# Kernel tuning notes

Measured on AMD Instinct MI355X. Metric: run time of the kernel, lower is better.

Reference implementation:

```python
import jax, jax.numpy as jnp
import numpy as np

MAX_ITERS = 20
TOL = 1e-3


def best_fit_transform(A, B):
    # A, B: [N, m]; returns homogeneous transform T mapping A -> B.
    m = A.shape[1]
    cA = jnp.mean(A, axis=0)
    cB = jnp.mean(B, axis=0)
    AA = A - cA
    BB = B - cB
    H = AA.T @ BB                      # [m, m] cross-covariance
    U, S, Vt = jnp.linalg.svd(H)
    # reflection fix: if det(R) < 0, flip last row of Vt
    R0 = Vt.T @ U.T
    flip = jnp.linalg.det(R0) < 0
    Vt = Vt.at[m - 1].multiply(jnp.where(flip, -1.0, 1.0).astype(Vt.dtype))
    R = Vt.T @ U.T
    t = cB - R @ cA
    T = jnp.eye(m + 1, dtype=A.dtype).at[:m, :m].set(R).at[:m, m].set(t)
    return T, R, t


def nearest_neighbor(src, dst):
    # src, dst: [N, m]; brute-force 1-NN of each src point in dst.
    d2 = (jnp.sum(src * src, axis=1)[:, None]
          - 2.0 * (src @ dst.T)
          + jnp.sum(dst * dst, axis=1)[None, :])        # [N, N]
    idx = jnp.argmin(d2, axis=1)                          # [N]
    dmin = jnp.take_along_axis(d2, idx[:, None], axis=1)[:, 0]
    dist = jnp.sqrt(jnp.maximum(dmin, 0.0) + 1e-12)
    return dist, idx


def icp(A, B, max_iterations=MAX_ITERS, tolerance=TOL):
    m = A.shape[1]
    N = A.shape[0]
    src0 = jnp.concatenate([A.T, jnp.ones((1, N), A.dtype)], axis=0)  # [m+1, N]

    def step(carry, _):
        src, prev_err, done = carry
        dist, idx = nearest_neighbor(src[:m].T, B)
        T, _, _ = best_fit_transform(src[:m].T, B[idx])
        new_src = T @ src
        err = jnp.mean(dist)
        converged = jnp.abs(prev_err - err) < tolerance
        src = jnp.where(done, src, new_src)
        prev_err = jnp.where(done, prev_err, err)
        done = done | converged
        return (src, prev_err, done), None

    carry0 = (src0, jnp.zeros((), A.dtype), jnp.zeros((), bool))
    (src, _, _), _ = jax.lax.scan(step, carry0, None, length=max_iterations)
    T, _, _ = best_fit_transform(A, src[:m].T)
    return T


def setup_inputs() -> dict:
    key = jax.random.key(0)
    kA, kB = jax.random.split(key)
    A = jax.random.normal(kA, (8192, 3), dtype=jnp.float32)
    B = jax.random.normal(kB, (8192, 3), dtype=jnp.float32)
    return {"A": A, "B": B}


def reference(A, B):
    return icp(A, B)
```

## Files before the change

kernel.cpp:

```cpp
#include <hip/hip_runtime.h>

#define NPTS   8192
#define NB     256
#define NT     256
#define NSTEP  (NPTS / 64)
#define MAXIT  20
#define TOLER  1e-3
#define SPINCAP 200000000u

typedef unsigned long long u64;
typedef unsigned int u32;

#define WS_PART    0
#define WS_FLAGS   65536

__device__ inline double atom_ld(const double* p) {
  return __hip_atomic_load(p, __ATOMIC_RELAXED, __HIP_MEMORY_SCOPE_AGENT);
}
__device__ inline void atom_st(double* p, double v) {
  __hip_atomic_store(p, v, __ATOMIC_RELAXED, __HIP_MEMORY_SCOPE_AGENT);
}
__device__ inline int atom_ldi(const int* p) {
  return __hip_atomic_load(p, __ATOMIC_RELAXED, __HIP_MEMORY_SCOPE_AGENT);
}
__device__ inline void atom_sti(int* p, int v) {
  __hip_atomic_store(p, v, __ATOMIC_RELAXED, __HIP_MEMORY_SCOPE_AGENT);
}

__device__ void eig3_sym_desc(const double K[3][3], double w[3], double V[3][3])
{
  const double p1 = K[0][1]*K[0][1] + K[0][2]*K[0][2] + K[1][2]*K[1][2];
  const double q  = (K[0][0] + K[1][1] + K[2][2]) / 3.0;
  const double p2 = (K[0][0]-q)*(K[0][0]-q) + (K[1][1]-q)*(K[1][1]-q)
                  + (K[2][2]-q)*(K[2][2]-q) + 2.0*p1;
  if (p2 < 1e-280) {
    w[0]=w[1]=w[2]=q;
    V[0][0]=1;V[1][0]=0;V[2][0]=0; V[0][1]=0;V[1][1]=1;V[2][1]=0;
    V[0][2]=0;V[1][2]=0;V[2][2]=1;
    return;
  }
  const double p = sqrt(p2 / 6.0);
  const double ip = 1.0 / p;
  double Bm[3][3];
  for (int i = 0; i < 3; ++i)
    for (int j = 0; j < 3; ++j)
      Bm[i][j] = (K[i][j] - ((i==j) ? q : 0.0)) * ip;
  double detB = Bm[0][0]*(Bm[1][1]*Bm[2][2] - Bm[1][2]*Bm[2][1])
              - Bm[0][1]*(Bm[1][0]*Bm[2][2] - Bm[1][2]*Bm[2][0])
              + Bm[0][2]*(Bm[1][0]*Bm[2][1] - Bm[1][1]*Bm[2][0]);
  double r = detB * 0.5;
  r = (r < -1.0) ? -1.0 : ((r > 1.0) ? 1.0 : r);
  const double phi = acos(r) / 3.0;
  w[0] = q + 2.0*p*cos(phi);
  w[2] = q + 2.0*p*cos(phi + 2.0943951023931953);
  w[1] = 3.0*q - w[0] - w[2];
  for (int kk = 0; kk < 2; ++kk) {
    const int k = (kk == 0) ? 0 : 2;
    double lam = w[k];
    double r0[3] = {K[0][0]-lam, K[0][1], K[0][2]};
    double r1[3] = {K[1][0], K[1][1]-lam, K[1][2]};
    double r2[3] = {K[2][0], K[2][1], K[2][2]-lam};
    double c01[3] = {r0[1]*r1[2]-r0[2]*r1[1], r0[2]*r1[0]-r0[0]*r1[2], r0[0]*r1[1]-r0[1]*r1[0]};
    double c12[3] = {r1[1]*r2[2]-r1[2]*r2[1], r1[2]*r2[0]-r1[0]*r2[2], r1[0]*r2[1]-r1[1]*r2[0]};
    double c20[3] = {r2[1]*r0[2]-r2[2]*r0[1], r2[2]*r0[0]-r2[0]*r0[2]*0 - r2[0]*r0[2] + r2[2]*r0[0]*0, 0};
    c20[0] = r2[1]*r0[2] - r2[2]*r0[1];
    c20[1] = r2[2]*r0[0] - r2[0]*r0[2];
    c20[2] = r2[0]*r0[1] - r2[1]*r0[0];
    double n01 = c01[0]*c01[0]+c01[1]*c01[1]+c01[2]*c01[2];
    double n12 = c12[0]*c12[0]+c12[1]*c12[1]+c12[2]*c12[2];
    double n20 = c20[0]*c20[0]+c20[1]*c20[1]+c20[2]*c20[2];
    double* best = c01; double nb = n01;
    if (n12 > nb) { best = c12; nb = n12; }
    if (n20 > nb) { best = c20; nb = n20; }
    double inv = 1.0 / sqrt(nb + 1e-300);
    V[0][k]=best[0]*inv; V[1][k]=best[1]*inv; V[2][k]=best[2]*inv;
  }
  V[0][1] = V[1][2]*V[2][0] - V[2][2]*V[1][0];
  V[1][1] = V[2][2]*V[0][0] - V[0][2]*V[2][0];
  V[2][1] = V[0][2]*V[1][0] - V[1][2]*V[0][0];
  double nm = sqrt(V[0][1]*V[0][1]+V[1][1]*V[1][1]+V[2][1]*V[2][1]) + 1e-300;
  V[0][1] /= nm; V[1][1] /= nm; V[2][1] /= nm;
}

__device__ void kabsch_R(const double H[3][3], double R[3][3])
{
  double K[3][3];
  for (int i = 0; i < 3; ++i)
    for (int j = 0; j < 3; ++j) {
      double s = 0.0;
      for (int k = 0; k < 3; ++k) s += H[k][i] * H[k][j];
      K[i][j] = s;
    }
  double w[3], V[3][3];
  eig3_sym_desc(K, w, V);
  double U[3][3];
  for (int k = 0; k < 3; ++k) {
    double u0 = H[0][0]*V[0][k] + H[0][1]*V[1][k] + H[0][2]*V[2][k];
    double u1 = H[1][0]*V[0][k] + H[1][1]*V[1][k] + H[1][2]*V[2][k];
    double u2 = H[2][0]*V[0][k] + H[2][1]*V[1][k] + H[2][2]*V[2][k];
    double n = sqrt(u0*u0 + u1*u1 + u2*u2);
    if (n > 1e-150) { u0 /= n; u1 /= n; u2 /= n; }
    else if (k == 2) {
      u0 = U[1][0]*U[2][1] - U[2][0]*U[1][1];
      u1 = U[2][0]*U[0][1] - U[0][0]*U[2][1];
      u2 = U[0][0]*U[1][1] - U[1][0]*U[0][1];
      double n2 = sqrt(u0*u0 + u1*u1 + u2*u2) + 1e-300;
      u0 /= n2; u1 /= n2; u2 /= n2;
    } else {
      u0 = (k == 0) ? 1.0 : 0.0; u1 = (k == 1) ? 1.0 : 0.0; u2 = 0.0;
    }
    U[0][k] = u0; U[1][k] = u1; U[2][k] = u2;
  }
  double R0[3][3];
  for (int i = 0; i < 3; ++i)
    for (int j = 0; j < 3; ++j)
      R0[i][j] = V[i][0]*U[j][0] + V[i][1]*U[j][1] + V[i][2]*U[j][2];
  double det = R0[0][0]*(R0[1][1]*R0[2][2] - R0[1][2]*R0[2][1])
             - R0[0][1]*(R0[1][0]*R0[2][2] - R0[1][2]*R0[2][0])
             + R0[0][2]*(R0[1][0]*R0[2][1] - R0[1][1]*R0[2][0]);
  if (det < 0.0)
    for (int i = 0; i < 3; ++i)
      for (int j = 0; j < 3; ++j)
        R0[i][j] -= 2.0 * V[i][2] * U[j][2];
  for (int i = 0; i < 3; ++i)
    for (int j = 0; j < 3; ++j)
      R[i][j] = R0[i][j];
}

__global__ void icp_init(char* __restrict__ ws)
{
  ((int*)(ws + WS_FLAGS))[threadIdx.x] = 0;
}

__device__ inline void flag_barrier(int* flags, int blk, int gen,
                                    int tid, int wav, int lane)
{
  __syncthreads();
  if (tid == 0) {
    __threadfence();
    atom_sti(&flags[blk], gen);
  }
  if (wav == 0) {
    const int base = lane * 4;
    u32 spins = 0;
    bool ok = false;
    while (!ok && spins < SPINCAP) {
      int f0 = atom_ldi(&flags[base + 0]);
      int f1 = atom_ldi(&flags[base + 1]);
      int f2 = atom_ldi(&flags[base + 2]);
      int f3 = atom_ldi(&flags[base + 3]);
      ok = __all((f0 >= gen) && (f1 >= gen) && (f2 >= gen) && (f3 >= gen));
      ++spins;
    }
  }
  __syncthreads();
  __threadfence();
}

__global__ __launch_bounds__(NT, 1)
void icp_all(const float* __restrict__ A, const float* __restrict__ B,
             char* __restrict__ ws, float* __restrict__ out)
{
  double* partials = (double*)(ws + WS_PART);
  int*    flags    = (int*)(ws + WS_FLAGS);

  __shared__ __align__(16) float4 bp_lds[NPTS];
  __shared__ double red1[32 * 16];
  __shared__ double red2[4 * 16];
  __shared__ float  Tl[12];
  __shared__ int    dl;

  const int tid  = threadIdx.x;
  const int blk  = blockIdx.x;
  const int wav  = tid >> 6;
  const int lane = tid & 63;
  const int qbase = blk * 32 + wav * 8;

  for (int i = tid; i < NPTS; i += NT) {
    float bx = B[3*i], by = B[3*i+1], bz = B[3*i+2];
    bp_lds[i] = make_float4(2.f*bx, 2.f*by, 2.f*bz, bx*bx + by*by + bz*bz);
  }

  float ax[8], ay[8], az[8], sx[8], sy[8], sz[8];
  #pragma unroll
  for (int i = 0; i < 8; ++i) {
    int p = qbase + i;
    ax[i] = A[3*p]; ay[i] = A[3*p+1]; az[i] = A[3*p+2];
    sx[i] = ax[i];  sy[i] = ay[i];    sz[i] = az[i];
  }
  __syncthreads();

  double prev_err = 0.0;
  int it = 0;
  for (; it < MAXIT; ++it) {
    const int par = it & 1;
    float emin[8]; int imin[8];
    #pragma unroll
    for (int i = 0; i < 8; ++i) { emin[i] = 3.4e38f; imin[i] = 0; }

    float4 dcur = bp_lds[lane];
    #pragma unroll 4
    for (int stp = 0; stp < NSTEP - 1; ++stp) {
      float4 dnxt = bp_lds[(stp + 1) * 64 + lane];
      const int jg = stp * 64 + lane;
      #pragma unroll
      for (int i = 0; i < 8; ++i) {
        float e = fmaf(-sx[i], dcur.x, fmaf(-sy[i], dcur.y, fmaf(-sz[i], dcur.z, dcur.w)));
        if (e < emin[i]) { emin[i] = e; imin[i] = jg; }
      }
      dcur = dnxt;
    }
    {
      const int jg = (NSTEP - 1) * 64 + lane;
      #pragma unroll
      for (int i = 0; i < 8; ++i) {
        float e = fmaf(-sx[i], dcur.x, fmaf(-sy[i], dcur.y, fmaf(-sz[i], dcur.z, dcur.w)));
        if (e < emin[i]) { emin[i] = e; imin[i] = jg; }
      }
    }
    #pragma unroll
    for (int m = 1; m < 64; m <<= 1) {
      #pragma unroll
      for (int i = 0; i < 8; ++i) {
        float eo = __shfl_xor(emin[i], m, 64);
        int   io = __shfl_xor(imin[i], m, 64);
        if (eo < emin[i] || (eo == emin[i] && io < imin[i])) { emin[i] = eo; imin[i] = io; }
      }
    }

    #pragma unroll
    for (int i = 0; i < 8; ++i) {
      if (lane == i) {
        float s2 = sx[i]*sx[i] + sy[i]*sy[i] + sz[i]*sz[i];
        float d2 = emin[i] + s2;
        float dist = sqrtf(fmaxf(d2, 0.f) + 1e-12f);
        int j = imin[i];
        float bx = B[3*j], by = B[3*j+1], bz = B[3*j+2];
        double* r = red1 + (wav * 8 + i) * 16;
        r[0]=sx[i]; r[1]=sy[i]; r[2]=sz[i];
        r[3]=bx;    r[4]=by;    r[5]=bz;
        r[6]=(double)sx[i]*bx;  r[7]=(double)sx[i]*by;  r[8]=(double)sx[i]*bz;
        r[9]=(double)sy[i]*bx;  r[10]=(double)sy[i]*by; r[11]=(double)sy[i]*bz;
        r[12]=(double)sz[i]*bx; r[13]=(double)sz[i]*by; r[14]=(double)sz[i]*bz;
        r[15]=dist;
      }
    }
    __syncthreads();
    if (tid < 16) {
      double ssum = 0.0;
      for (int g = 0; g < 32; ++g) ssum += red1[g * 16 + tid];
      atom_st(&partials[((size_t)par * 16 + tid) * NB + blk], ssum);
    }
    flag_barrier(flags, blk, it + 1, tid, wav, lane);

    {
      double a2[16];
      #pragma unroll
      for (int k = 0; k < 16; ++k)
        a2[k] = atom_ld(&partials[((size_t)par * 16 + k) * NB + tid]);
      for (int m = 1; m < 64; m <<= 1) {
        #pragma unroll
        for (int k = 0; k < 16; ++k) a2[k] += __shfl_xor(a2[k], m, 64);
      }
      if (lane == 0)
        for (int k = 0; k < 16; ++k) red2[wav * 16 + k] = a2[k];
    }
    __syncthreads();
    if (tid == 0) {
      double S[16];
      for (int k = 0; k < 16; ++k)
        S[k] = red2[k] + red2[16+k] + red2[32+k] + red2[48+k];
      const double invN = 1.0 / NPTS;
      double cAv[3] = {S[0]*invN, S[1]*invN, S[2]*invN};
      double cBv[3] = {S[3]*invN, S[4]*invN, S[5]*invN};
      double H[3][3];
      for (int i = 0; i < 3; ++i)
        for (int j = 0; j < 3; ++j)
          H[i][j] = S[6 + i*3 + j] - (double)NPTS * cAv[i] * cBv[j];
      double err = S[15] * invN;
      int conv = (fabs(prev_err - err) < TOLER) ? 1 : 0;
      prev_err = err;
      double R[3][3];
      kabsch_R(H, R);
      double t0 = cBv[0] - (R[0][0]*cAv[0] + R[0][1]*cAv[1] + R[0][2]*cAv[2]);
      double t1 = cBv[1] - (R[1][0]*cAv[0] + R[1][1]*cAv[1] + R[1][2]*cAv[2]);
      double t2 = cBv[2] - (R[2][0]*cAv[0] + R[2][1]*cAv[1] + R[2][2]*cAv[2]);
      Tl[0]=(float)R[0][0]; Tl[1]=(float)R[0][1]; Tl[2]=(float)R[0][2];
      Tl[3]=(float)R[1][0]; Tl[4]=(float)R[1][1]; Tl[5]=(float)R[1][2];
      Tl[6]=(float)R[2][0]; Tl[7]=(float)R[2][1]; Tl[8]=(float)R[2][2];
      Tl[9]=(float)t0; Tl[10]=(float)t1; Tl[11]=(float)t2;
      dl = conv;
    }
    __syncthreads();
    {
      float r00=Tl[0],r01=Tl[1],r02=Tl[2],r10=Tl[3],r11=Tl[4],r12=Tl[5];
      float r20=Tl[6],r21=Tl[7],r22=Tl[8],t0=Tl[9],t1=Tl[10],t2=Tl[11];
      int done = dl;
      #pragma unroll
      for (int i = 0; i < 8; ++i) {
        float nx = r00*sx[i] + r01*sy[i] + r02*sz[i] + t0;
        float ny = r10*sx[i] + r11*sy[i] + r12*sz[i] + t1;
        float nz = r20*sx[i] + r21*sy[i] + r22*sz[i] + t2;
        sx[i]=nx; sy[i]=ny; sz[i]=nz;
      }
      if (done) break;
    }
  }

  const int  fpar = (it < MAXIT) ? ((it + 1) & 1) : (MAXIT & 1);
  const int  fgen = (it < MAXIT) ? (it + 2) : (MAXIT + 1);
  __syncthreads();
  #pragma unroll
  for (int i = 0; i < 8; ++i) {
    if (lane == i) {
      double* r = red1 + (wav * 8 + i) * 16;
      r[0]=ax[i]; r[1]=ay[i]; r[2]=az[i];
      r[3]=sx[i]; r[4]=sy[i]; r[5]=sz[i];
      r[6]=(double)ax[i]*sx[i];  r[7]=(double)ax[i]*sy[i];  r[8]=(double)ax[i]*sz[i];
      r[9]=(double)ay[i]*sx[i];  r[10]=(double)ay[i]*sy[i]; r[11]=(double)ay[i]*sz[i];
      r[12]=(double)az[i]*sx[i]; r[13]=(double)az[i]*sy[i]; r[14]=(double)az[i]*sz[i];
      r[15]=0.0;
    }
  }
  __syncthreads();
  if (tid < 16) {
    double ssum = 0.0;
    for (int g = 0; g < 32; ++g) ssum += red1[g * 16 + tid];
    atom_st(&partials[((size_t)fpar * 16 + tid) * NB + blk], ssum);
  }
  if (blk != 0) {
    __syncthreads();
    if (tid == 0) { __threadfence(); atom_sti(&flags[blk], fgen); }
    return;
  }
  flag_barrier(flags, blk, fgen, tid, wav, lane);

  double a2[16];
  #pragma unroll
  for (int k = 0; k < 16; ++k)
    a2[k] = atom_ld(&partials[((size_t)fpar * 16 + k) * NB + tid]);
  for (int m = 1; m < 64; m <<= 1) {
    #pragma unroll
    for (int k = 0; k < 16; ++k) a2[k] += __shfl_xor(a2[k], m, 64);
  }
  if (lane == 0)
    for (int k = 0; k < 16; ++k) red2[wav * 16 + k] = a2[k];
  __syncthreads();
  if (tid == 0) {
    double S[16];
    for (int k = 0; k < 16; ++k)
      S[k] = red2[k] + red2[16+k] + red2[32+k] + red2[48+k];
    const double invN = 1.0 / NPTS;
    double cAv[3] = {S[0]*invN, S[1]*invN, S[2]*invN};
    double cSv[3] = {S[3]*invN, S[4]*invN, S[5]*invN};
    double H[3][3];
    for (int i = 0; i < 3; ++i)
      for (int j = 0; j < 3; ++j)
        H[i][j] = S[6 + i*3 + j] - (double)NPTS * cAv[i] * cSv[j];
    double R[3][3];
    kabsch_R(H, R);
    double u0 = cSv[0] - (R[0][0]*cAv[0] + R[0][1]*cAv[1] + R[0][2]*cAv[2]);
    double u1 = cSv[1] - (R[1][0]*cAv[0] + R[1][1]*cAv[1] + R[1][2]*cAv[2]);
    double u2 = cSv[2] - (R[2][0]*cAv[0] + R[2][1]*cAv[1] + R[2][2]*cAv[2]);
    out[0]=(float)R[0][0]; out[1]=(float)R[0][1]; out[2]=(float)R[0][2]; out[3]=(float)u0;
    out[4]=(float)R[1][0]; out[5]=(float)R[1][1]; out[6]=(float)R[1][2]; out[7]=(float)u1;
    out[8]=(float)R[2][0]; out[9]=(float)R[2][1]; out[10]=(float)R[2][2]; out[11]=(float)u2;
    out[12]=0.f; out[13]=0.f; out[14]=0.f; out[15]=1.f;
  }
}

extern "C" void kernel_launch(void* const* d_in, const int* in_sizes, int n_in,
                              void* d_out, int out_size, void* d_ws, size_t ws_size,
                              hipStream_t stream) {
  const float* A = (const float*)d_in[0];
  const float* B = (const float*)d_in[1];
  float* out = (float*)d_out;
  char* ws = (char*)d_ws;

  hipLaunchKernelGGL(icp_init, dim3(1), dim3(NT), 0, stream, ws);
  hipLaunchKernelGGL(icp_all, dim3(NB), dim3(NT), 0, stream, A, B, ws, out);
}
```

Measured before the change: 171.3 us.

## Use 512 threads with 4 sources per wave and float Kabsch solve

Doubles the block size to 512 threads and halves the number of source points each wave handles (8 to 4). Each block still covers 32 points, but with 8 waves per CU instead of 4, giving more latency hiding in the NN scan. The per-iteration 3x3 eigen/Kabsch solve on the serial critical path now runs in float instead of double, to cut the latency of the single-thread step between grid barriers. Only the first four waves do the partial-sum reduction, and the init kernel now launches NB threads. The trade-offs are possible loss of precision in the rotation and more waves taking part in each barrier.

```diff
diff --git a/kernel.cpp b/kernel.cpp
--- a/kernel.cpp
+++ b/kernel.cpp
@@ -2,7 +2,8 @@
 
 #define NPTS   8192
 #define NB     256
-#define NT     256
+#define NT     512
+#define SRCW   4
 #define NSTEP  (NPTS / 64)
 #define MAXIT  20
 #define TOLER  1e-3
@@ -27,101 +28,98 @@
   __hip_atomic_store(p, v, __ATOMIC_RELAXED, __HIP_MEMORY_SCOPE_AGENT);
 }
 
-__device__ void eig3_sym_desc(const double K[3][3], double w[3], double V[3][3])
-{
-  const double p1 = K[0][1]*K[0][1] + K[0][2]*K[0][2] + K[1][2]*K[1][2];
-  const double q  = (K[0][0] + K[1][1] + K[2][2]) / 3.0;
-  const double p2 = (K[0][0]-q)*(K[0][0]-q) + (K[1][1]-q)*(K[1][1]-q)
-                  + (K[2][2]-q)*(K[2][2]-q) + 2.0*p1;
-  if (p2 < 1e-280) {
+__device__ void eig3f(const float K[3][3], float w[3], float V[3][3])
+{
+  const float p1 = K[0][1]*K[0][1] + K[0][2]*K[0][2] + K[1][2]*K[1][2];
+  const float q  = (K[0][0] + K[1][1] + K[2][2]) * (1.f/3.f);
+  const float p2 = (K[0][0]-q)*(K[0][0]-q) + (K[1][1]-q)*(K[1][1]-q)
+                 + (K[2][2]-q)*(K[2][2]-q) + 2.f*p1;
+  if (p2 < 1e-20f) {
     w[0]=w[1]=w[2]=q;
     V[0][0]=1;V[1][0]=0;V[2][0]=0; V[0][1]=0;V[1][1]=1;V[2][1]=0;
     V[0][2]=0;V[1][2]=0;V[2][2]=1;
     return;
   }
-  const double p = sqrt(p2 / 6.0);
-  const double ip = 1.0 / p;
-  double Bm[3][3];
+  const float p = sqrtf(p2 * (1.f/6.f));
+  const float ip = 1.f / p;
+  float Bm[3][3];
   for (int i = 0; i < 3; ++i)
     for (int j = 0; j < 3; ++j)
-      Bm[i][j] = (K[i][j] - ((i==j) ? q : 0.0)) * ip;
-  double detB = Bm[0][0]*(Bm[1][1]*Bm[2][2] - Bm[1][2]*Bm[2][1])
-              - Bm[0][1]*(Bm[1][0]*Bm[2][2] - Bm[1][2]*Bm[2][0])
-              + Bm[0][2]*(Bm[1][0]*Bm[2][1] - Bm[1][1]*Bm[2][0]);
-  double r = detB * 0.5;
-  r = (r < -1.0) ? -1.0 : ((r > 1.0) ? 1.0 : r);
-  const double phi = acos(r) / 3.0;
-  w[0] = q + 2.0*p*cos(phi);
-  w[2] = q + 2.0*p*cos(phi + 2.0943951023931953);
-  w[1] = 3.0*q - w[0] - w[2];
+      Bm[i][j] = (K[i][j] - ((i==j) ? q : 0.f)) * ip;
+  float detB = Bm[0][0]*(Bm[1][1]*Bm[2][2] - Bm[1][2]*Bm[2][1])
+             - Bm[0][1]*(Bm[1][0]*Bm[2][2] - Bm[1][2]*Bm[2][0])
+             + Bm[0][2]*(Bm[1][0]*Bm[2][1] - Bm[1][1]*Bm[2][0]);
+  float r = detB * 0.5f;
+  r = fminf(1.f, fmaxf(-1.f, r));
+  const float phi = acosf(r) * (1.f/3.f);
+  w[0] = q + 2.f*p*cosf(phi);
+  w[2] = q + 2.f*p*cosf(phi + 2.0943951023931953f);
+  w[1] = 3.f*q - w[0] - w[2];
   for (int kk = 0; kk < 2; ++kk) {
     const int k = (kk == 0) ? 0 : 2;
-    double lam = w[k];
-    double r0[3] = {K[0][0]-lam, K[0][1], K[0][2]};
-    double r1[3] = {K[1][0], K[1][1]-lam, K[1][2]};
-    double r2[3] = {K[2][0], K[2][1], K[2][2]-lam};
-    double c01[3] = {r0[1]*r1[2]-r0[2]*r1[1], r0[2]*r1[0]-r0[0]*r1[2], r0[0]*r1[1]-r0[1]*r1[0]};
-    double c12[3] = {r1[1]*r2[2]-r1[2]*r2[1], r1[2]*r2[0]-r1[0]*r2[2], r1[0]*r2[1]-r1[1]*r2[0]};
-    double c20[3] = {r2[1]*r0[2]-r2[2]*r0[1], r2[2]*r0[0]-r2[0]*r0[2]*0 - r2[0]*r0[2] + r2[2]*r0[0]*0, 0};
-    c20[0] = r2[1]*r0[2] - r2[2]*r0[1];
-    c20[1] = r2[2]*r0[0] - r2[0]*r0[2];
-    c20[2] = r2[0]*r0[1] - r2[1]*r0[0];
-    double n01 = c01[0]*c01[0]+c01[1]*c01[1]+c01[2]*c01[2];
-    double n12 = c12[0]*c12[0]+c12[1]*c12[1]+c12[2]*c12[2];
-    double n20 = c20[0]*c20[0]+c20[1]*c20[1]+c20[2]*c20[2];
-    double* best = c01; double nb = n01;
+    float lam = w[k];
+    float r0[3] = {K[0][0]-lam, K[0][1], K[0][2]};
+    float r1[3] = {K[1][0], K[1][1]-lam, K[1][2]};
+    float r2[3] = {K[2][0], K[2][1], K[2][2]-lam};
+    float c01[3] = {r0[1]*r1[2]-r0[2]*r1[1], r0[2]*r1[0]-r0[0]*r1[2], r0[0]*r1[1]-r0[1]*r1[0]};
+    float c12[3] = {r1[1]*r2[2]-r1[2]*r2[1], r1[2]*r2[0]-r1[0]*r2[2], r1[0]*r2[1]-r1[1]*r2[0]};
+    float c20[3] = {r2[1]*r0[2]-r2[2]*r0[1], r2[2]*r0[0]-r2[0]*r0[2], r2[0]*r0[1]-r2[1]*r0[0]};
+    float n01 = c01[0]*c01[0]+c01[1]*c01[1]+c01[2]*c01[2];
+    float n12 = c12[0]*c12[0]+c12[1]*c12[1]+c12[2]*c12[2];
+    float n20 = c20[0]*c20[0]+c20[1]*c20[1]+c20[2]*c20[2];
+    float* best = c01; float nb = n01;
     if (n12 > nb) { best = c12; nb = n12; }
     if (n20 > nb) { best = c20; nb = n20; }
-    double inv = 1.0 / sqrt(nb + 1e-300);
+    float inv = 1.f / sqrtf(nb + 1e-30f);
     V[0][k]=best[0]*inv; V[1][k]=best[1]*inv; V[2][k]=best[2]*inv;
   }
   V[0][1] = V[1][2]*V[2][0] - V[2][2]*V[1][0];
   V[1][1] = V[2][2]*V[0][0] - V[0][2]*V[2][0];
   V[2][1] = V[0][2]*V[1][0] - V[1][2]*V[0][0];
-  double nm = sqrt(V[0][1]*V[0][1]+V[1][1]*V[1][1]+V[2][1]*V[2][1]) + 1e-300;
+  float nm = sqrtf(V[0][1]*V[0][1]+V[1][1]*V[1][1]+V[2][1]*V[2][1]) + 1e-30f;
   V[0][1] /= nm; V[1][1] /= nm; V[2][1] /= nm;
 }
 
-__device__ void kabsch_R(const double H[3][3], double R[3][3])
-{
-  double K[3][3];
+__device__ void kabsch_Rf(const float H[3][3], float R[3][3])
+{
+  float K[3][3];
   for (int i = 0; i < 3; ++i)
     for (int j = 0; j < 3; ++j) {
-      double s = 0.0;
+      float s = 0.f;
       for (int k = 0; k < 3; ++k) s += H[k][i] * H[k][j];
       K[i][j] = s;
     }
-  double w[3], V[3][3];
-  eig3_sym_desc(K, w, V);
-  double U[3][3];
+  float w[3], V[3][3];
+  eig3f(K, w, V);
+  float U[3][3];
   for (int k = 0; k < 3; ++k) {
-    double u0 = H[0][0]*V[0][k] + H[0][1]*V[1][k] + H[0][2]*V[2][k];
-    double u1 = H[1][0]*V[0][k] + H[1][1]*V[1][k] + H[1][2]*V[2][k];
-    double u2 = H[2][0]*V[0][k] + H[2][1]*V[1][k] + H[2][2]*V[2][k];
-    double n = sqrt(u0*u0 + u1*u1 + u2*u2);
-    if (n > 1e-150) { u0 /= n; u1 /= n; u2 /= n; }
+    float u0 = H[0][0]*V[0][k] + H[0][1]*V[1][k] + H[0][2]*V[2][k];
+    float u1 = H[1][0]*V[0][k] + H[1][1]*V[1][k] + H[1][2]*V[2][k];
+    float u2 = H[2][0]*V[0][k] + H[2][1]*V[1][k] + H[2][2]*V[2][k];
+    float n = sqrtf(u0*u0 + u1*u1 + u2*u2);
+    if (n > 1e-18f) { u0 /= n; u1 /= n; u2 /= n; }
     else if (k == 2) {
       u0 = U[1][0]*U[2][1] - U[2][0]*U[1][1];
       u1 = U[2][0]*U[0][1] - U[0][0]*U[2][1];
       u2 = U[0][0]*U[1][1] - U[1][0]*U[0][1];
-      double n2 = sqrt(u0*u0 + u1*u1 + u2*u2) + 1e-300;
+      float n2 = sqrtf(u0*u0 + u1*u1 + u2*u2) + 1e-30f;
       u0 /= n2; u1 /= n2; u2 /= n2;
     } else {
-      u0 = (k == 0) ? 1.0 : 0.0; u1 = (k == 1) ? 1.0 : 0.0; u2 = 0.0;
+      u0 = (k == 0) ? 1.f : 0.f; u1 = (k == 1) ? 1.f : 0.f; u2 = 0.f;
     }
     U[0][k] = u0; U[1][k] = u1; U[2][k] = u2;
   }
-  double R0[3][3];
+  float R0[3][3];
   for (int i = 0; i < 3; ++i)
     for (int j = 0; j < 3; ++j)
       R0[i][j] = V[i][0]*U[j][0] + V[i][1]*U[j][1] + V[i][2]*U[j][2];
-  double det = R0[0][0]*(R0[1][1]*R0[2][2] - R0[1][2]*R0[2][1])
-             - R0[0][1]*(R0[1][0]*R0[2][2] - R0[1][2]*R0[2][0])
-             + R0[0][2]*(R0[1][0]*R0[2][1] - R0[1][1]*R0[2][0]);
-  if (det < 0.0)
+  float det = R0[0][0]*(R0[1][1]*R0[2][2] - R0[1][2]*R0[2][1])
+            - R0[0][1]*(R0[1][0]*R0[2][2] - R0[1][2]*R0[2][0])
+            + R0[0][2]*(R0[1][0]*R0[2][1] - R0[1][1]*R0[2][0]);
+  if (det < 0.f)
     for (int i = 0; i < 3; ++i)
       for (int j = 0; j < 3; ++j)
-        R0[i][j] -= 2.0 * V[i][2] * U[j][2];
+        R0[i][j] -= 2.f * V[i][2] * U[j][2];
   for (int i = 0; i < 3; ++i)
     for (int j = 0; j < 3; ++j)
       R[i][j] = R0[i][j];
@@ -174,16 +172,16 @@
   const int blk  = blockIdx.x;
   const int wav  = tid >> 6;
   const int lane = tid & 63;
-  const int qbase = blk * 32 + wav * 8;
+  const int qbase = blk * 32 + wav * SRCW;
 
   for (int i = tid; i < NPTS; i += NT) {
     float bx = B[3*i], by = B[3*i+1], bz = B[3*i+2];
     bp_lds[i] = make_float4(2.f*bx, 2.f*by, 2.f*bz, bx*bx + by*by + bz*bz);
   }
 
-  float ax[8], ay[8], az[8], sx[8], sy[8], sz[8];
+  float ax[SRCW], ay[SRCW], az[SRCW], sx[SRCW], sy[SRCW], sz[SRCW];
   #pragma unroll
-  for (int i = 0; i < 8; ++i) {
+  for (int i = 0; i < SRCW; ++i) {
     int p = qbase + i;
     ax[i] = A[3*p]; ay[i] = A[3*p+1]; az[i] = A[3*p+2];
     sx[i] = ax[i];  sy[i] = ay[i];    sz[i] = az[i];
@@ -194,9 +192,9 @@
   int it = 0;
   for (; it < MAXIT; ++it) {
     const int par = it & 1;
-    float emin[8]; int imin[8];
+    float emin[SRCW]; int imin[SRCW];
     #pragma unroll
-    for (int i = 0; i < 8; ++i) { emin[i] = 3.4e38f; imin[i] = 0; }
+    for (int i = 0; i < SRCW; ++i) { emin[i] = 3.4e38f; imin[i] = 0; }
 
     float4 dcur = bp_lds[lane];
     #pragma unroll 4
@@ -204,7 +202,7 @@
       float4 dnxt = bp_lds[(stp + 1) * 64 + lane];
       const int jg = stp * 64 + lane;
       #pragma unroll
-      for (int i = 0; i < 8; ++i) {
+      for (int i = 0; i < SRCW; ++i) {
         float e = fmaf(-sx[i], dcur.x, fmaf(-sy[i], dcur.y, fmaf(-sz[i], dcur.z, dcur.w)));
         if (e < emin[i]) { emin[i] = e; imin[i] = jg; }
       }
@@ -213,7 +211,7 @@
     {
       const int jg = (NSTEP - 1) * 64 + lane;
       #pragma unroll
-      for (int i = 0; i < 8; ++i) {
+      for (int i = 0; i < SRCW; ++i) {
         float e = fmaf(-sx[i], dcur.x, fmaf(-sy[i], dcur.y, fmaf(-sz[i], dcur.z, dcur.w)));
         if (e < emin[i]) { emin[i] = e; imin[i] = jg; }
       }
@@ -221,7 +219,7 @@
     #pragma unroll
     for (int m = 1; m < 64; m <<= 1) {
       #pragma unroll
-      for (int i = 0; i < 8; ++i) {
+      for (int i = 0; i < SRCW; ++i) {
         float eo = __shfl_xor(emin[i], m, 64);
         int   io = __shfl_xor(imin[i], m, 64);
         if (eo < emin[i] || (eo == emin[i] && io < imin[i])) { emin[i] = eo; imin[i] = io; }
@@ -229,14 +227,14 @@
     }
 
     #pragma unroll
-    for (int i = 0; i < 8; ++i) {
+    for (int i = 0; i < SRCW; ++i) {
       if (lane == i) {
         float s2 = sx[i]*sx[i] + sy[i]*sy[i] + sz[i]*sz[i];
         float d2 = emin[i] + s2;
         float dist = sqrtf(fmaxf(d2, 0.f) + 1e-12f);
         int j = imin[i];
         float bx = B[3*j], by = B[3*j+1], bz = B[3*j+2];
-        double* r = red1 + (wav * 8 + i) * 16;
+        double* r = red1 + (wav * SRCW + i) * 16;
         r[0]=sx[i]; r[1]=sy[i]; r[2]=sz[i];
         r[3]=bx;    r[4]=by;    r[5]=bz;
         r[6]=(double)sx[i]*bx;  r[7]=(double)sx[i]*by;  r[8]=(double)sx[i]*bz;
@@ -253,7 +251,7 @@
     }
     flag_barrier(flags, blk, it + 1, tid, wav, lane);
 
-    {
+    if (wav < 4) {
       double a2[16];
       #pragma unroll
       for (int k = 0; k < 16; ++k)
@@ -273,22 +271,22 @@
       const double invN = 1.0 / NPTS;
       double cAv[3] = {S[0]*invN, S[1]*invN, S[2]*invN};
       double cBv[3] = {S[3]*invN, S[4]*invN, S[5]*invN};
-      double H[3][3];
+      float H[3][3];
       for (int i = 0; i < 3; ++i)
         for (int j = 0; j < 3; ++j)
-          H[i][j] = S[6 + i*3 + j] - (double)NPTS * cAv[i] * cBv[j];
+          H[i][j] = (float)(S[6 + i*3 + j] - (double)NPTS * cAv[i] * cBv[j]);
       double err = S[15] * invN;
       int conv = (fabs(prev_err - err) < TOLER) ? 1 : 0;
       prev_err = err;
-      double R[3][3];
-      kabsch_R(H, R);
-      double t0 = cBv[0] - (R[0][0]*cAv[0] + R[0][1]*cAv[1] + R[0][2]*cAv[2]);
-      double t1 = cBv[1] - (R[1][0]*cAv[0] + R[1][1]*cAv[1] + R[1][2]*cAv[2]);
-      double t2 = cBv[2] - (R[2][0]*cAv[0] + R[2][1]*cAv[1] + R[2][2]*cAv[2]);
-      Tl[0]=(float)R[0][0]; Tl[1]=(float)R[0][1]; Tl[2]=(float)R[0][2];
-      Tl[3]=(float)R[1][0]; Tl[4]=(float)R[1][1]; Tl[5]=(float)R[1][2];
-      Tl[6]=(float)R[2][0]; Tl[7]=(float)R[2][1]; Tl[8]=(float)R[2][2];
-      Tl[9]=(float)t0; Tl[10]=(float)t1; Tl[11]=(float)t2;
+      float R[3][3];
+      kabsch_Rf(H, R);
+      float t0 = (float)cBv[0] - (R[0][0]*(float)cAv[0] + R[0][1]*(float)cAv[1] + R[0][2]*(float)cAv[2]);
+      float t1 = (float)cBv[1] - (R[1][0]*(float)cAv[0] + R[1][1]*(float)cAv[1] + R[1][2]*(float)cAv[2]);
+      float t2 = (float)cBv[2] - (R[2][0]*(float)cAv[0] + R[2][1]*(float)cAv[1] + R[2][2]*(float)cAv[2]);
+      Tl[0]=R[0][0]; Tl[1]=R[0][1]; Tl[2]=R[0][2];
+      Tl[3]=R[1][0]; Tl[4]=R[1][1]; Tl[5]=R[1][2];
+      Tl[6]=R[2][0]; Tl[7]=R[2][1]; Tl[8]=R[2][2];
+      Tl[9]=t0; Tl[10]=t1; Tl[11]=t2;
       dl = conv;
     }
     __syncthreads();
@@ -297,7 +295,7 @@
       float r20=Tl[6],r21=Tl[7],r22=Tl[8],t0=Tl[9],t1=Tl[10],t2=Tl[11];
       int done = dl;
       #pragma unroll
-      for (int i = 0; i < 8; ++i) {
+      for (int i = 0; i < SRCW; ++i) {
         float nx = r00*sx[i] + r01*sy[i] + r02*sz[i] + t0;
         float ny = r10*sx[i] + r11*sy[i] + r12*sz[i] + t1;
         float nz = r20*sx[i] + r21*sy[i] + r22*sz[i] + t2;
@@ -311,9 +309,9 @@
   const int  fgen = (it < MAXIT) ? (it + 2) : (MAXIT + 1);
   __syncthreads();
   #pragma unroll
-  for (int i = 0; i < 8; ++i) {
+  for (int i = 0; i < SRCW; ++i) {
     if (lane == i) {
-      double* r = red1 + (wav * 8 + i) * 16;
+      double* r = red1 + (wav * SRCW + i) * 16;
       r[0]=ax[i]; r[1]=ay[i]; r[2]=az[i];
       r[3]=sx[i]; r[4]=sy[i]; r[5]=sz[i];
       r[6]=(double)ax[i]*sx[i];  r[7]=(double)ax[i]*sy[i];  r[8]=(double)ax[i]*sz[i];
@@ -335,16 +333,18 @@
   }
   flag_barrier(flags, blk, fgen, tid, wav, lane);
 
-  double a2[16];
-  #pragma unroll
-  for (int k = 0; k < 16; ++k)
-    a2[k] = atom_ld(&partials[((size_t)fpar * 16 + k) * NB + tid]);
-  for (int m = 1; m < 64; m <<= 1) {
+  if (wav < 4) {
+    double a2[16];
     #pragma unroll
-    for (int k = 0; k < 16; ++k) a2[k] += __shfl_xor(a2[k], m, 64);
-  }
-  if (lane == 0)
-    for (int k = 0; k < 16; ++k) red2[wav * 16 + k] = a2[k];
+    for (int k = 0; k < 16; ++k)
+      a2[k] = atom_ld(&partials[((size_t)fpar * 16 + k) * NB + tid]);
+    for (int m = 1; m < 64; m <<= 1) {
+      #pragma unroll
+      for (int k = 0; k < 16; ++k) a2[k] += __shfl_xor(a2[k], m, 64);
+    }
+    if (lane == 0)
+      for (int k = 0; k < 16; ++k) red2[wav * 16 + k] = a2[k];
+  }
   __syncthreads();
   if (tid == 0) {
     double S[16];
@@ -353,18 +353,18 @@
     const double invN = 1.0 / NPTS;
     double cAv[3] = {S[0]*invN, S[1]*invN, S[2]*invN};
     double cSv[3] = {S[3]*invN, S[4]*invN, S[5]*invN};
-    double H[3][3];
+    float H[3][3];
     for (int i = 0; i < 3; ++i)
       for (int j = 0; j < 3; ++j)
-        H[i][j] = S[6 + i*3 + j] - (double)NPTS * cAv[i] * cSv[j];
-    double R[3][3];
-    kabsch_R(H, R);
-    double u0 = cSv[0] - (R[0][0]*cAv[0] + R[0][1]*cAv[1] + R[0][2]*cAv[2]);
-    double u1 = cSv[1] - (R[1][0]*cAv[0] + R[1][1]*cAv[1] + R[1][2]*cAv[2]);
-    double u2 = cSv[2] - (R[2][0]*cAv[0] + R[2][1]*cAv[1] + R[2][2]*cAv[2]);
-    out[0]=(float)R[0][0]; out[1]=(float)R[0][1]; out[2]=(float)R[0][2]; out[3]=(float)u0;
-    out[4]=(float)R[1][0]; out[5]=(float)R[1][1]; out[6]=(float)R[1][2]; out[7]=(float)u1;
-    out[8]=(float)R[2][0]; out[9]=(float)R[2][1]; out[10]=(float)R[2][2]; out[11]=(float)u2;
+        H[i][j] = (float)(S[6 + i*3 + j] - (double)NPTS * cAv[i] * cSv[j]);
+    float R[3][3];
+    kabsch_Rf(H, R);
+    float u0 = (float)cSv[0] - (R[0][0]*(float)cAv[0] + R[0][1]*(float)cAv[1] + R[0][2]*(float)cAv[2]);
+    float u1 = (float)cSv[1] - (R[1][0]*(float)cAv[0] + R[1][1]*(float)cAv[1] + R[1][2]*(float)cAv[2]);
+    float u2 = (float)cSv[2] - (R[2][0]*(float)cAv[0] + R[2][1]*(float)cAv[1] + R[2][2]*(float)cAv[2]);
+    out[0]=R[0][0]; out[1]=R[0][1]; out[2]=R[0][2]; out[3]=u0;
+    out[4]=R[1][0]; out[5]=R[1][1]; out[6]=R[1][2]; out[7]=u1;
+    out[8]=R[2][0]; out[9]=R[2][1]; out[10]=R[2][2]; out[11]=u2;
     out[12]=0.f; out[13]=0.f; out[14]=0.f; out[15]=1.f;
   }
 }
@@ -377,6 +377,6 @@
   float* out = (float*)d_out;
   char* ws = (char*)d_ws;
 
-  hipLaunchKernelGGL(icp_init, dim3(1), dim3(NT), 0, stream, ws);
+  hipLaunchKernelGGL(icp_init, dim3(1), dim3(NB), 0, stream, ws);
   hipLaunchKernelGGL(icp_all, dim3(NB), dim3(NT), 0, stream, A, B, ws, out);
 }
```

Result: slower. 177.7 us (+3.7%).
